# Optimization experiments

Hardware: AMD Instinct MI355X
Metric: run time of the kernel (lower is better)

The kernel has to match this reference:

```python
import jax, jax.numpy as jnp
import numpy as np

ALPHA = 0.5            # conf['alpha'] hybrid mixing
MAX_TOP_ANT = 50       # conf['max_top_antecedents']
MAX_SPAN_WIDTH = 30


def bucket_distance(d):
    # util.bucket_distance: identity 0..4, then log2 buckets, clipped to [0, 9]
    logspace = jnp.floor(jnp.log2(jnp.maximum(d, 1).astype(jnp.float32))).astype(d.dtype) + 3
    return jnp.clip(jnp.where(d <= 4, d, logspace), 0, 9)


def setup_inputs() -> dict:
    key = jax.random.key(0)
    ks = jax.random.split(key, 16)
    W, D, K, F, H = 4096, 768, 768, 20, 1000
    SPAN = 3 * D                      # span_emb_size = 3 * bert_emb_size
    PAIR = 3 * SPAN + F               # pair_emb_size (use_features only)
    std = 0.02

    mention_doc = jax.random.normal(ks[0], (W, D), jnp.float32)
    mention_doc_one = jax.random.normal(ks[1], (W, D), jnp.float32)
    top_span_starts = jnp.sort(jax.random.randint(ks[2], (K,), 0, W - MAX_SPAN_WIDTH))
    widths = jax.random.randint(ks[3], (K,), 0, MAX_SPAN_WIDTH)
    top_span_ends = jnp.minimum(top_span_starts + widths, W - 1)
    top_span_mention_scores = jax.random.normal(ks[4], (K,), jnp.float32)

    return {
        "mention_doc": mention_doc,
        "mention_doc_one": mention_doc_one,
        "top_span_starts": top_span_starts,
        "top_span_ends": top_span_ends,
        "top_span_mention_scores": top_span_mention_scores,
        # mention_token_attn: Linear(D -> 1)
        "attn_w": jax.random.normal(ks[5], (D,), jnp.float32) * std,
        "attn_b": jnp.zeros((), jnp.float32),
        # coarse_bilinear: Linear(SPAN -> SPAN)
        "coarse_w": jax.random.normal(ks[6], (SPAN, SPAN), jnp.float32) * std,
        "coarse_b": jnp.zeros((SPAN,), jnp.float32),
        # emb_antecedent_distance_prior [10, F] + antecedent_distance_score_ffnn Linear(F -> 1)
        "dist_prior_emb": jax.random.normal(ks[7], (10, F), jnp.float32) * std,
        "dist_w": jax.random.normal(ks[8], (F,), jnp.float32) * std,
        "dist_b": jnp.zeros((), jnp.float32),
        # emb_top_antecedent_distance [10, F]
        "top_dist_emb": jax.random.normal(ks[9], (10, F), jnp.float32) * std,
        # coref_score_ffnn: Linear(PAIR -> H), ReLU, Linear(H -> 1)
        "coref_w1": jax.random.normal(ks[10], (PAIR, H), jnp.float32) * std,
        "coref_b1": jnp.zeros((H,), jnp.float32),
        "coref_w2": jax.random.normal(ks[11], (H,), jnp.float32) * std,
        "coref_b2": jnp.zeros((), jnp.float32),
    }


def reference(mention_doc, mention_doc_one, top_span_starts, top_span_ends,
              top_span_mention_scores, attn_w, attn_b, coarse_w, coarse_b,
              dist_prior_emb, dist_w, dist_b, top_dist_emb,
              coref_w1, coref_b1, coref_w2, coref_b2):
    W = mention_doc.shape[0]
    K = top_span_starts.shape[0]
    C = min(K, MAX_TOP_ANT)
    NEG_INF = jnp.float32(-1e30) * 0 - jnp.inf  # true -inf, matches torch.log(0.)

    # --- span embeddings: start / end / head-attention over hybrid doc ---
    start_emb = mention_doc[top_span_starts]                      # [K, D]
    end_emb = mention_doc[top_span_ends]                          # [K, D]
    hybrid = mention_doc * (1.0 - ALPHA) + mention_doc_one * ALPHA
    token_attn = hybrid @ attn_w + attn_b                         # [W]
    tok = jnp.arange(W)
    span_tok_mask = (tok[None, :] >= top_span_starts[:, None]) & \
                    (tok[None, :] <= top_span_ends[:, None])      # [K, W]
    attn_raw = jnp.where(span_tok_mask, token_attn[None, :], NEG_INF)
    attn_probs = jax.nn.softmax(attn_raw, axis=1)                 # [K, W]
    head_emb = attn_probs @ hybrid                                # [K, D]
    span_emb = jnp.concatenate([start_emb, end_emb, head_emb], axis=1)  # [K, 3D]

    # --- coarse (fast) pairwise scores ---
    rng = jnp.arange(K)
    ant_offsets = rng[:, None] - rng[None, :]                     # [K, K]
    ant_mask = ant_offsets >= 1
    pair_sum = top_span_mention_scores[:, None] + top_span_mention_scores[None, :]
    src = span_emb @ coarse_w + coarse_b                          # coarse_bilinear
    fast = pair_sum + src @ span_emb.T
    fast = jnp.where(ant_mask, fast, NEG_INF)                     # + log(mask)
    dist_score = dist_prior_emb @ dist_w + dist_b                 # [10]
    fast = fast + dist_score[bucket_distance(ant_offsets)]        # distance prior

    # --- top-k antecedent pruning ---
    top_fast, top_idx = jax.lax.top_k(fast, C)                    # [K, C]
    top_ant_offsets = jnp.take_along_axis(ant_offsets, top_idx, axis=1)

    # --- fine-grained pairwise FFNN scoring ---
    dist_emb = top_dist_emb[bucket_distance(top_ant_offsets)]     # [K, C, F]
    ant_emb = span_emb[top_idx]                                   # [K, C, 3D]
    tgt_emb = jnp.broadcast_to(span_emb[:, None, :], ant_emb.shape)
    sim_emb = span_emb[:, None, :] * ant_emb
    pair_emb = jnp.concatenate([tgt_emb, ant_emb, sim_emb, dist_emb], axis=-1)  # [K, C, PAIR]
    h = jax.nn.relu(jnp.einsum('kcp,ph->kch', pair_emb, coref_w1) + coref_b1)
    slow = jnp.einsum('kch,h->kc', h, coref_w2) + coref_b2        # [K, C]
    top_scores = slow + top_fast

    # dummy antecedent (epsilon) column of zeros
    return jnp.concatenate([jnp.zeros((K, 1), top_scores.dtype), top_scores], axis=1)
```

## Files before the change

### kernel.cpp

```cpp
#include <hip/hip_runtime.h>
#include <math.h>

#define WTOK 4096
#define DD   768
#define KK   768
#define SPAN 2304
#define HH   1000
#define CC   50
#define NPAD 1024
#define NBIG 4352

typedef __attribute__((ext_vector_type(8))) short bf16x8;
typedef __attribute__((ext_vector_type(4))) float f32x4;
typedef unsigned short ushort;
typedef unsigned int uint;

__device__ __forceinline__ int bucketd(int d) {
  int l = (d >= 1) ? (31 - __clz(d)) : 0;
  int v = (d <= 4) ? d : (l + 3);
  return min(max(v, 0), 9);
}
__device__ __forceinline__ ushort f2bf(float f) {
  uint u = __float_as_uint(f);
  return (ushort)((u + 0x7fffu + ((u >> 16) & 1u)) >> 16);
}
__device__ __forceinline__ uint pkmul_t(uint a, uint b) {
  float lo = __uint_as_float(a << 16) * __uint_as_float(b << 16);
  float hi = __uint_as_float(a & 0xffff0000u) * __uint_as_float(b & 0xffff0000u);
  return (__float_as_uint(lo) >> 16) | (__float_as_uint(hi) & 0xffff0000u);
}
__device__ __forceinline__ uint4 pkmul4(uint4 a, uint4 b) {
  uint4 r;
  r.x = pkmul_t(a.x, b.x); r.y = pkmul_t(a.y, b.y);
  r.z = pkmul_t(a.z, b.z); r.w = pkmul_t(a.w, b.w);
  return r;
}
__device__ __forceinline__ void dma16(const ushort* g, ushort* l) {
  __builtin_amdgcn_global_load_lds(
      (const __attribute__((address_space(1))) void*)g,
      (__attribute__((address_space(3))) void*)l, 16, 0, 0);
}

#define PB_COARSE 5184
#define PB_W 2304
#define PB_SETUP_BASE (PB_COARSE + 3 * PB_W)
#define PB_SLOW_BASE  (PB_SETUP_BASE + 40)
#define PB_TOTAL      (PB_SLOW_BASE + 150)

__global__ __launch_bounds__(256) void prep_k(
    const float* __restrict__ coarse_w, const float* __restrict__ W1,
    const float* __restrict__ dist_prior, const float* __restrict__ dist_w,
    const float* __restrict__ dist_b, const float* __restrict__ top_dist,
    ushort* __restrict__ BigT, ushort* __restrict__ W1simT,
    float* __restrict__ dist_score, float* __restrict__ Pdist,
    float* __restrict__ slow)
{
  int bid = blockIdx.x;
  int tid = threadIdx.x;
  if (bid >= PB_SLOW_BASE) {
    int t = (bid - PB_SLOW_BASE) * 256 + tid;
    if (t < KK * CC) slow[t] = 0.f;
    return;
  }
  if (bid >= PB_SETUP_BASE) {
    int t = (bid - PB_SETUP_BASE) * 256 + tid;
    if (t < 10) {
      float s = dist_b[0];
      for (int f = 0; f < 20; ++f) s += dist_prior[t * 20 + f] * dist_w[f];
      dist_score[t] = s;
    }
    if (t < 10 * HH) {
      int b = t / HH, h = t % HH;
      float s = 0.f;
      for (int f = 0; f < 20; ++f)
        s += top_dist[b * 20 + f] * W1[(long)(6912 + f) * HH + h];
      Pdist[t] = s;
    }
    return;
  }
  const float* in; int ldin, Cin, nbase, NBrows; ushort* out; int idx;
  int xt;
  if (bid < PB_COARSE) {
    idx = bid; in = coarse_w; ldin = SPAN; Cin = SPAN; nbase = 0;
    NBrows = NBIG; out = BigT; xt = SPAN / 32;
  } else {
    idx = bid - PB_COARSE;
    int region = idx / PB_W;
    idx = idx % PB_W;
    if (region == 0) { in = W1; nbase = 2304; NBrows = NBIG; out = BigT; }
    else if (region == 1) { in = W1 + (size_t)SPAN * HH; nbase = 3328; NBrows = NBIG; out = BigT; }
    else { in = W1 + (size_t)2 * SPAN * HH; nbase = 0; NBrows = NPAD; out = W1simT; }
    ldin = HH; Cin = HH; xt = NPAD / 32;
  }
  {
    int bx = idx % xt, by = idx / xt;
    __shared__ float tile[32][33];
    int n0 = bx * 32, p0 = by * 32;
    int tx = tid & 31, ty = tid >> 5;
    for (int i = ty; i < 32; i += 8) {
      int p = p0 + i, n = n0 + tx;
      tile[i][tx] = (n < Cin) ? in[(long)p * ldin + n] : 0.f;
    }
    __syncthreads();
    size_t slab = (size_t)(p0 >> 5) * NBrows * 32;
    for (int i = ty; i < 32; i += 8) {
      int n = n0 + i;
      out[slab + (size_t)(nbase + n) * 32 + tx] = f2bf(tile[tx][i]);
    }
  }
}

__global__ __launch_bounds__(256) void hybrid_attn_k(
    const float* __restrict__ doc, const float* __restrict__ doc1,
    const float* __restrict__ attn_w, const float* __restrict__ attn_b,
    float* __restrict__ hybrid, float* __restrict__ tok_attn)
{
  int w = blockIdx.x;
  int tid = threadIdx.x;
  float part = 0.f;
  for (int d = tid; d < DD; d += 256) {
    float h = 0.5f * doc[(long)w * DD + d] + 0.5f * doc1[(long)w * DD + d];
    hybrid[(long)w * DD + d] = h;
    part += h * attn_w[d];
  }
  for (int off = 32; off > 0; off >>= 1) part += __shfl_down(part, off, 64);
  __shared__ float ws4[4];
  if ((tid & 63) == 0) ws4[tid >> 6] = part;
  __syncthreads();
  if (tid == 0) tok_attn[w] = ws4[0] + ws4[1] + ws4[2] + ws4[3] + attn_b[0];
}

__global__ __launch_bounds__(256) void span_emb_k(
    const float* __restrict__ doc, const float* __restrict__ hybrid,
    const float* __restrict__ tok_attn, const int* __restrict__ starts,
    const int* __restrict__ ends, ushort* __restrict__ se_bf)
{
  int k = blockIdx.x;
  int s = starts[k], e = ends[k];
  int len = e - s + 1;
  int tid = threadIdx.x;
  __shared__ float p_s[32];
  if (tid < 32) {
    float v = (tid < len) ? tok_attn[s + tid] : -INFINITY;
    float m = v;
    for (int msk = 16; msk >= 1; msk >>= 1) m = fmaxf(m, __shfl_xor(m, msk, 32));
    float pe = (tid < len) ? expf(v - m) : 0.f;
    float Z = pe;
    for (int msk = 16; msk >= 1; msk >>= 1) Z += __shfl_xor(Z, msk, 32);
    p_s[tid] = pe / Z;
  }
  __syncthreads();
  for (int d = tid; d < DD; d += 256) {
    float h = 0.f;
    for (int t = 0; t < len; ++t) h += p_s[t] * hybrid[(long)(s + t) * DD + d];
    se_bf[(long)k * SPAN + d]          = f2bf(doc[(long)s * DD + d]);
    se_bf[(long)k * SPAN + DD + d]     = f2bf(doc[(long)e * DD + d]);
    se_bf[(long)k * SPAN + 2 * DD + d] = f2bf(h);
  }
}

__global__ __launch_bounds__(256) void gemm_combined_k(
    const ushort* __restrict__ A, const ushort* __restrict__ B,
    const float* __restrict__ coarse_b, const float* __restrict__ b1,
    ushort* __restrict__ src_bf, float* __restrict__ Ptgt,
    float* __restrict__ Pant)
{
  __shared__ __align__(16) ushort As[64 * 40];
  __shared__ __align__(16) ushort Bs[128 * 32];
  int tid = threadIdx.x;
  int m0 = blockIdx.x * 64, n0 = blockIdx.y * 128;
  int lane = tid & 63, wid = tid >> 6;
  int quad = lane >> 4, lr = lane & 15;
  int wm = (wid & 1) << 5, wn = (wid >> 1) << 6;
  int arow = tid >> 2, aq = tid & 3;
  int gofs[2];
#pragma unroll
  for (int t = 0; t < 2; ++t) {
    int S = t * 256 + tid;
    int r = S >> 2, p = S & 3;
    int q = p ^ ((r >> 1) & 3);
    gofs[t] = (n0 + r) * 32 + q * 8;
  }
  f32x4 acc[2][4] = {};
  for (int k0 = 0; k0 < SPAN; k0 += 32) {
    uint4 a0 = *(const uint4*)(A + (size_t)(m0 + arow) * SPAN + k0 + aq * 8);
    __syncthreads();
    const ushort* sb = B + (size_t)(k0 >> 5) * (NBIG * 32);
    dma16(sb + gofs[0], &Bs[(size_t)(0 * 256 + tid) * 8]);
    dma16(sb + gofs[1], &Bs[(size_t)(1 * 256 + tid) * 8]);
    *(uint4*)&As[arow * 40 + aq * 8] = a0;
    __syncthreads();
    bf16x8 af[2], bfr[4];
#pragma unroll
    for (int mi = 0; mi < 2; ++mi)
      af[mi] = *(const bf16x8*)&As[(wm + mi * 16 + lr) * 40 + quad * 8];
#pragma unroll
    for (int ni = 0; ni < 4; ++ni) {
      int r = wn + ni * 16 + lr;
      int p = quad ^ ((r >> 1) & 3);
      bfr[ni] = *(const bf16x8*)&Bs[r * 32 + p * 8];
    }
#pragma unroll
    for (int mi = 0; mi < 2; ++mi)
#pragma unroll
      for (int ni = 0; ni < 4; ++ni)
        acc[mi][ni] = __builtin_amdgcn_mfma_f32_16x16x32_bf16(
            af[mi], bfr[ni], acc[mi][ni], 0, 0, 0);
  }
#pragma unroll
  for (int mi = 0; mi < 2; ++mi)
#pragma unroll
    for (int ni = 0; ni < 4; ++ni) {
      f32x4 c = acc[mi][ni];
#pragma unroll
      for (int reg = 0; reg < 4; ++reg) {
        int gm = m0 + wm + mi * 16 + quad * 4 + reg;
        int g = n0 + wn + ni * 16 + lr;
        float v = c[reg];
        if (g < 2304) {
          src_bf[(size_t)gm * SPAN + g] = f2bf(v + coarse_b[g]);
        } else if (g < 3328) {
          int n = g - 2304;
          if (n < HH) Ptgt[(size_t)gm * HH + n] = v + b1[n];
        } else {
          int n = g - 3328;
          if (n < HH) Pant[(size_t)gm * HH + n] = v;
        }
      }
    }
}

__global__ __launch_bounds__(256) void gemm_fast_k(
    const ushort* __restrict__ A, const ushort* __restrict__ B,
    const float* __restrict__ ms, const float* __restrict__ dist_score,
    float* __restrict__ fast)
{
  __shared__ __align__(16) ushort As[64 * 40];
  __shared__ __align__(16) ushort Bs[64 * 40];
  int tid = threadIdx.x;
  int m0 = blockIdx.x * 64, n0 = blockIdx.y * 64;
  int lane = tid & 63, wid = tid >> 6;
  int quad = lane >> 4, lr = lane & 15;
  int wm = (wid & 1) << 5, wn = (wid >> 1) << 5;
  int row = tid >> 2, aq = tid & 3;
  const ushort* ga = A + (size_t)(m0 + row) * SPAN + aq * 8;
  const ushort* gb = B + (size_t)(n0 + row) * SPAN + aq * 8;
  f32x4 acc[2][2] = {};
  for (int k0 = 0; k0 < SPAN; k0 += 32) {
    uint4 a0 = *(const uint4*)(ga + k0);
    uint4 b0 = *(const uint4*)(gb + k0);
    __syncthreads();
    *(uint4*)&As[row * 40 + aq * 8] = a0;
    *(uint4*)&Bs[row * 40 + aq * 8] = b0;
    __syncthreads();
    bf16x8 af[2], bfr[2];
#pragma unroll
    for (int mi = 0; mi < 2; ++mi)
      af[mi] = *(const bf16x8*)&As[(wm + mi * 16 + lr) * 40 + quad * 8];
#pragma unroll
    for (int ni = 0; ni < 2; ++ni)
      bfr[ni] = *(const bf16x8*)&Bs[(wn + ni * 16 + lr) * 40 + quad * 8];
#pragma unroll
    for (int mi = 0; mi < 2; ++mi)
#pragma unroll
      for (int ni = 0; ni < 2; ++ni)
        acc[mi][ni] = __builtin_amdgcn_mfma_f32_16x16x32_bf16(
            af[mi], bfr[ni], acc[mi][ni], 0, 0, 0);
  }
#pragma unroll
  for (int mi = 0; mi < 2; ++mi)
#pragma unroll
    for (int ni = 0; ni < 2; ++ni) {
      f32x4 c = acc[mi][ni];
#pragma unroll
      for (int reg = 0; reg < 4; ++reg) {
        int gm = m0 + wm + mi * 16 + quad * 4 + reg;
        int gn = n0 + wn + ni * 16 + lr;
        float v;
        if (gn < gm) {
          v = c[reg] + ms[gm] + ms[gn] + dist_score[bucketd(gm - gn)];
        } else {
          v = -INFINITY;
        }
        fast[(size_t)gm * KK + gn] = v;
      }
    }
}

__global__ __launch_bounds__(256) void topk_k(
    const float* __restrict__ fast, float* __restrict__ top_fast,
    int* __restrict__ row_j, int* __restrict__ row_bucket)
{
  __shared__ float vals[KK];
  __shared__ float wbv[4];
  __shared__ int wbi[4];
  int k = blockIdx.x;
  int tid = threadIdx.x;
  for (int j = tid; j < KK; j += 256) vals[j] = fast[(long)k * KK + j];
  __syncthreads();
  const float NANF = __uint_as_float(0x7fc00000u);
  for (int it = 0; it < CC; ++it) {
    float bv = -INFINITY;
    int bi = 1 << 30;
    for (int j = tid; j < KK; j += 256) {
      float v = vals[j];
      if (v > bv || (v == bv && j < bi)) { bv = v; bi = j; }
    }
    for (int off = 32; off > 0; off >>= 1) {
      float ov = __shfl_down(bv, off, 64);
      int oi = __shfl_down(bi, off, 64);
      if (ov > bv || (ov == bv && oi < bi)) { bv = ov; bi = oi; }
    }
    if ((tid & 63) == 0) { wbv[tid >> 6] = bv; wbi[tid >> 6] = bi; }
    __syncthreads();
    if (tid == 0) {
      for (int w = 1; w < 4; ++w) {
        float ov = wbv[w]; int oi = wbi[w];
        if (ov > bv || (ov == bv && oi < bi)) { bv = ov; bi = oi; }
      }
      int r = k * CC + it;
      top_fast[r] = bv;
      row_j[r] = bi;
      row_bucket[r] = bucketd(k - bi);
      vals[bi] = NANF;
    }
    __syncthreads();
  }
}

__global__ __launch_bounds__(256, 4) void pair_mfma_k(
    const ushort* __restrict__ se_bf, const ushort* __restrict__ W1simT,
    const int* __restrict__ row_j, const int* __restrict__ row_bucket,
    const float* __restrict__ Ptgt, const float* __restrict__ Pant,
    const float* __restrict__ Pdist, const float* __restrict__ w2,
    float* __restrict__ slow)
{
  __shared__ __align__(16) ushort As[2][128 * 40];
  __shared__ __align__(16) ushort Bs[2][128 * 32];
  __shared__ int ks_s[128];
  __shared__ int js_s[128];
  __shared__ int bk_s[128];
  int tid = threadIdx.x;
  int m0 = blockIdx.x * 128, n0 = blockIdx.y * 128;
  if (tid < 128) {
    int r = m0 + tid;
    ks_s[tid] = r / CC;
    js_s[tid] = row_j[r];
    bk_s[tid] = row_bucket[r];
  }
  __syncthreads();
  int lane = tid & 63, wid = tid >> 6;
  int quad = lane >> 4, lr = lane & 15;
  int wm = (wid & 1) << 6, wn = (wid >> 1) << 6;
  int ar0 = tid >> 2, aq = tid & 3;
  const ushort* pk0 = se_bf + (size_t)ks_s[ar0] * SPAN + aq * 8;
  const ushort* pj0 = se_bf + (size_t)js_s[ar0] * SPAN + aq * 8;
  const ushort* pk1 = se_bf + (size_t)ks_s[ar0 + 64] * SPAN + aq * 8;
  const ushort* pj1 = se_bf + (size_t)js_s[ar0 + 64] * SPAN + aq * 8;
  int gofs[2];
#pragma unroll
  for (int t = 0; t < 2; ++t) {
    int S = t * 256 + tid;
    int r = S >> 2, p = S & 3;
    int q = p ^ ((r >> 1) & 3);
    gofs[t] = (n0 + r) * 32 + q * 8;
  }

  {
    uint4 ka0 = *(const uint4*)(pk0);
    uint4 ja0 = *(const uint4*)(pj0);
    uint4 ka1 = *(const uint4*)(pk1);
    uint4 ja1 = *(const uint4*)(pj1);
#pragma unroll
    for (int t = 0; t < 2; ++t)
      dma16(W1simT + gofs[t], &Bs[0][(size_t)(t * 256 + tid) * 8]);
    *(uint4*)&As[0][ar0 * 40 + aq * 8]        = pkmul4(ka0, ja0);
    *(uint4*)&As[0][(ar0 + 64) * 40 + aq * 8] = pkmul4(ka1, ja1);
  }
  __syncthreads();

  f32x4 acc[4][4] = {};
  for (int k0 = 0; k0 < SPAN; k0 += 32) {
    int buf = (k0 >> 5) & 1, nb = buf ^ 1;
    bool more = (k0 + 32) < SPAN;
    int k1 = more ? k0 + 32 : k0;
    uint4 ka0 = *(const uint4*)(pk0 + k1);
    uint4 ja0 = *(const uint4*)(pj0 + k1);
    uint4 ka1 = *(const uint4*)(pk1 + k1);
    uint4 ja1 = *(const uint4*)(pj1 + k1);
    if (more) {
      const ushort* sb = W1simT + (size_t)(k1 >> 5) * (NPAD * 32);
#pragma unroll
      for (int t = 0; t < 2; ++t)
        dma16(sb + gofs[t], &Bs[nb][(size_t)(t * 256 + tid) * 8]);
    }
    bf16x8 af[4], bfr[4];
#pragma unroll
    for (int mi = 0; mi < 4; ++mi)
      af[mi] = *(const bf16x8*)&As[buf][(wm + mi * 16 + lr) * 40 + quad * 8];
#pragma unroll
    for (int ni = 0; ni < 4; ++ni) {
      int r = wn + ni * 16 + lr;
      int p = quad ^ ((r >> 1) & 3);
      bfr[ni] = *(const bf16x8*)&Bs[buf][r * 32 + p * 8];
    }
#pragma unroll
    for (int ni = 0; ni < 4; ++ni)
#pragma unroll
      for (int mi = 0; mi < 4; ++mi)
        acc[mi][ni] = __builtin_amdgcn_mfma_f32_16x16x32_bf16(
            af[mi], bfr[ni], acc[mi][ni], 0, 0, 0);
    if (more) {
      *(uint4*)&As[nb][ar0 * 40 + aq * 8]        = pkmul4(ka0, ja0);
      *(uint4*)&As[nb][(ar0 + 64) * 40 + aq * 8] = pkmul4(ka1, ja1);
    }
    __syncthreads();
  }
  int nn[4]; float w2r[4]; bool nv[4];
#pragma unroll
  for (int ni = 0; ni < 4; ++ni) {
    nn[ni] = n0 + wn + ni * 16 + lr;
    nv[ni] = nn[ni] < HH;
    w2r[ni] = nv[ni] ? w2[nn[ni]] : 0.f;
  }
#pragma unroll
  for (int mi = 0; mi < 4; ++mi) {
#pragma unroll
    for (int reg = 0; reg < 4; ++reg) {
      int rl = wm + mi * 16 + quad * 4 + reg;
      int kk = ks_s[rl], jj = js_s[rl], bb = bk_s[rl];
      float s = 0.f;
#pragma unroll
      for (int ni = 0; ni < 4; ++ni) {
        if (nv[ni]) {
          float h = acc[mi][ni][reg] + Ptgt[(size_t)kk * HH + nn[ni]] +
                    Pant[(size_t)jj * HH + nn[ni]] +
                    Pdist[(size_t)bb * HH + nn[ni]];
          s += fmaxf(h, 0.f) * w2r[ni];
        }
      }
      s += __shfl_xor(s, 1); s += __shfl_xor(s, 2);
      s += __shfl_xor(s, 4); s += __shfl_xor(s, 8);
      if (lr == 0) atomicAdd(&slow[m0 + rl], s);
    }
  }
}

__global__ void finalize_k(const float* __restrict__ slow,
                           const float* __restrict__ top_fast,
                           const float* __restrict__ b2, float* __restrict__ out)
{
  int t = blockIdx.x * 256 + threadIdx.x;
  if (t >= KK * (CC + 1)) return;
  int k = t / (CC + 1), col = t % (CC + 1);
  if (col == 0) {
    out[t] = 0.f;
  } else {
    int r = k * CC + col - 1;
    float v = slow[r] + b2[0] + top_fast[r];
    if (!isfinite(v)) v = -1.0e30f;
    out[t] = v;
  }
}

extern "C" void kernel_launch(void* const* d_in, const int* in_sizes, int n_in,
                              void* d_out, int out_size, void* d_ws, size_t ws_size,
                              hipStream_t stream)
{
  const float* doc        = (const float*)d_in[0];
  const float* doc1       = (const float*)d_in[1];
  const int*   starts     = (const int*)d_in[2];
  const int*   ends       = (const int*)d_in[3];
  const float* ms         = (const float*)d_in[4];
  const float* attn_w     = (const float*)d_in[5];
  const float* attn_b     = (const float*)d_in[6];
  const float* coarse_w   = (const float*)d_in[7];
  const float* coarse_b   = (const float*)d_in[8];
  const float* dist_prior = (const float*)d_in[9];
  const float* dist_w     = (const float*)d_in[10];
  const float* dist_b     = (const float*)d_in[11];
  const float* top_dist   = (const float*)d_in[12];
  const float* W1         = (const float*)d_in[13];
  const float* b1         = (const float*)d_in[14];
  const float* w2         = (const float*)d_in[15];
  const float* b2         = (const float*)d_in[16];
  float* out = (float*)d_out;

  char* ws = (char*)d_ws;
  size_t off = 0;
  auto alloc = [&](size_t bytes) { void* p = ws + off; off = (off + bytes + 1023) & ~(size_t)1023; return p; };
  float*  hybrid     = (float*)alloc((size_t)WTOK * DD * 4);
  float*  tok_attn   = (float*)alloc((size_t)WTOK * 4);
  ushort* se_bf      = (ushort*)alloc((size_t)KK * SPAN * 2 + 4096);
  ushort* src_bf     = (ushort*)alloc((size_t)KK * SPAN * 2 + 4096);
  float*  fast       = (float*)alloc((size_t)KK * KK * 4);
  float*  Ptgt       = (float*)alloc((size_t)KK * HH * 4);
  float*  Pant       = (float*)alloc((size_t)KK * HH * 4);
  float*  Pdist      = (float*)alloc((size_t)10 * HH * 4);
  float*  dist_score = (float*)alloc(64);
  float*  top_fast   = (float*)alloc((size_t)KK * CC * 4);
  int*    row_j      = (int*)alloc((size_t)KK * CC * 4);
  int*    row_bucket = (int*)alloc((size_t)KK * CC * 4);
  float*  slow       = (float*)alloc((size_t)KK * CC * 4);
  ushort* BigT       = (ushort*)alloc((size_t)NBIG * SPAN * 2 + 4096);
  ushort* W1simT     = (ushort*)alloc((size_t)NPAD * SPAN * 2 + 4096);
  (void)ws_size; (void)in_sizes; (void)n_in; (void)out_size;

  prep_k<<<PB_TOTAL, 256, 0, stream>>>(coarse_w, W1, dist_prior, dist_w,
                                       dist_b, top_dist, BigT, W1simT,
                                       dist_score, Pdist, slow);
  hybrid_attn_k<<<WTOK, 256, 0, stream>>>(doc, doc1, attn_w, attn_b, hybrid, tok_attn);
  span_emb_k<<<KK, 256, 0, stream>>>(doc, hybrid, tok_attn, starts, ends, se_bf);
  {
    dim3 g(KK / 64, NBIG / 128);
    gemm_combined_k<<<g, 256, 0, stream>>>(se_bf, BigT, coarse_b, b1,
                                           src_bf, Ptgt, Pant);
  }
  {
    dim3 g(KK / 64, KK / 64);
    gemm_fast_k<<<g, 256, 0, stream>>>(src_bf, se_bf, ms, dist_score, fast);
  }
  topk_k<<<KK, 256, 0, stream>>>(fast, top_fast, row_j, row_bucket);
  {
    dim3 g((KK * CC) / 128, NPAD / 128);
    pair_mfma_k<<<g, 256, 0, stream>>>(se_bf, W1simT, row_j, row_bucket,
                                       Ptgt, Pant, Pdist, w2, slow);
  }
  finalize_k<<<(KK * (CC + 1) + 255) / 256, 256, 0, stream>>>(slow, top_fast, b2, out);
}
```

Baseline: 562.5 us.

## Precompute pairwise product operand in k-tiled layout and DMA it in pair GEMM

The elementwise product of target and antecedent span embeddings now comes from a separate prod_k kernel. It writes the product into a k-tiled bf16 buffer, in two passes of 19200 rows each, instead of the pair GEMM computing it on the fly from gathered rows. The pair GEMM then loads both A and B tiles with async DMA into swizzled LDS, which removes per-iteration register gathers and packed multiplies from the main loop. In exchange it writes and rereads roughly 88MB per pass, and the pair GEMM launches go from one to two.

```diff
diff --git a/kernel.cpp b/kernel.cpp
--- a/kernel.cpp
+++ b/kernel.cpp
@@ -9,6 +9,7 @@
 #define CC   50
 #define NPAD 1024
 #define NBIG 4352
+#define MP   19200
 
 typedef __attribute__((ext_vector_type(8))) short bf16x8;
 typedef __attribute__((ext_vector_type(4))) float f32x4;
@@ -328,14 +329,36 @@
   }
 }
 
+__global__ __launch_bounds__(256) void prod_k(
+    const ushort* __restrict__ se_bf, const int* __restrict__ row_j,
+    int mbase, ushort* __restrict__ A_kt)
+{
+  int tid = threadIdx.x;
+  int m0 = blockIdx.x * 128;
+  int s = blockIdx.y;
+  int row = tid >> 2, aq = tid & 3;
+#pragma unroll
+  for (int h = 0; h < 2; ++h) {
+    int ml = m0 + row + h * 64;
+    int g = mbase + ml;
+    int kk = g / CC;
+    int jj = row_j[g];
+    uint4 a = *(const uint4*)(se_bf + (size_t)kk * SPAN + s * 32 + aq * 8);
+    uint4 b = *(const uint4*)(se_bf + (size_t)jj * SPAN + s * 32 + aq * 8);
+    *(uint4*)(A_kt + (size_t)s * (MP * 32) + (size_t)ml * 32 + aq * 8) =
+        pkmul4(a, b);
+  }
+}
+
 __global__ __launch_bounds__(256, 4) void pair_mfma_k(
-    const ushort* __restrict__ se_bf, const ushort* __restrict__ W1simT,
+    const ushort* __restrict__ A_kt, const ushort* __restrict__ W1simT,
     const int* __restrict__ row_j, const int* __restrict__ row_bucket,
+    int mbase,
     const float* __restrict__ Ptgt, const float* __restrict__ Pant,
     const float* __restrict__ Pdist, const float* __restrict__ w2,
     float* __restrict__ slow)
 {
-  __shared__ __align__(16) ushort As[2][128 * 40];
+  __shared__ __align__(16) ushort As[2][128 * 32];
   __shared__ __align__(16) ushort Bs[2][128 * 32];
   __shared__ int ks_s[128];
   __shared__ int js_s[128];
@@ -343,39 +366,28 @@
   int tid = threadIdx.x;
   int m0 = blockIdx.x * 128, n0 = blockIdx.y * 128;
   if (tid < 128) {
-    int r = m0 + tid;
-    ks_s[tid] = r / CC;
-    js_s[tid] = row_j[r];
-    bk_s[tid] = row_bucket[r];
-  }
-  __syncthreads();
+    int g = mbase + m0 + tid;
+    ks_s[tid] = g / CC;
+    js_s[tid] = row_j[g];
+    bk_s[tid] = row_bucket[g];
+  }
   int lane = tid & 63, wid = tid >> 6;
   int quad = lane >> 4, lr = lane & 15;
   int wm = (wid & 1) << 6, wn = (wid >> 1) << 6;
-  int ar0 = tid >> 2, aq = tid & 3;
-  const ushort* pk0 = se_bf + (size_t)ks_s[ar0] * SPAN + aq * 8;
-  const ushort* pj0 = se_bf + (size_t)js_s[ar0] * SPAN + aq * 8;
-  const ushort* pk1 = se_bf + (size_t)ks_s[ar0 + 64] * SPAN + aq * 8;
-  const ushort* pj1 = se_bf + (size_t)js_s[ar0 + 64] * SPAN + aq * 8;
-  int gofs[2];
+  int aofs[2], bofs[2];
 #pragma unroll
   for (int t = 0; t < 2; ++t) {
     int S = t * 256 + tid;
     int r = S >> 2, p = S & 3;
     int q = p ^ ((r >> 1) & 3);
-    gofs[t] = (n0 + r) * 32 + q * 8;
-  }
-
-  {
-    uint4 ka0 = *(const uint4*)(pk0);
-    uint4 ja0 = *(const uint4*)(pj0);
-    uint4 ka1 = *(const uint4*)(pk1);
-    uint4 ja1 = *(const uint4*)(pj1);
-#pragma unroll
-    for (int t = 0; t < 2; ++t)
-      dma16(W1simT + gofs[t], &Bs[0][(size_t)(t * 256 + tid) * 8]);
-    *(uint4*)&As[0][ar0 * 40 + aq * 8]        = pkmul4(ka0, ja0);
-    *(uint4*)&As[0][(ar0 + 64) * 40 + aq * 8] = pkmul4(ka1, ja1);
+    aofs[t] = (m0 + r) * 32 + q * 8;
+    bofs[t] = (n0 + r) * 32 + q * 8;
+  }
+
+#pragma unroll
+  for (int t = 0; t < 2; ++t) {
+    dma16(A_kt + aofs[t], &As[0][(size_t)(t * 256 + tid) * 8]);
+    dma16(W1simT + bofs[t], &Bs[0][(size_t)(t * 256 + tid) * 8]);
   }
   __syncthreads();
 
@@ -383,21 +395,23 @@
   for (int k0 = 0; k0 < SPAN; k0 += 32) {
     int buf = (k0 >> 5) & 1, nb = buf ^ 1;
     bool more = (k0 + 32) < SPAN;
-    int k1 = more ? k0 + 32 : k0;
-    uint4 ka0 = *(const uint4*)(pk0 + k1);
-    uint4 ja0 = *(const uint4*)(pj0 + k1);
-    uint4 ka1 = *(const uint4*)(pk1 + k1);
-    uint4 ja1 = *(const uint4*)(pj1 + k1);
     if (more) {
-      const ushort* sb = W1simT + (size_t)(k1 >> 5) * (NPAD * 32);
-#pragma unroll
-      for (int t = 0; t < 2; ++t)
-        dma16(sb + gofs[t], &Bs[nb][(size_t)(t * 256 + tid) * 8]);
+      int s1 = (k0 >> 5) + 1;
+      const ushort* sa = A_kt + (size_t)s1 * (MP * 32);
+      const ushort* sb = W1simT + (size_t)s1 * (NPAD * 32);
+#pragma unroll
+      for (int t = 0; t < 2; ++t) {
+        dma16(sa + aofs[t], &As[nb][(size_t)(t * 256 + tid) * 8]);
+        dma16(sb + bofs[t], &Bs[nb][(size_t)(t * 256 + tid) * 8]);
+      }
     }
     bf16x8 af[4], bfr[4];
 #pragma unroll
-    for (int mi = 0; mi < 4; ++mi)
-      af[mi] = *(const bf16x8*)&As[buf][(wm + mi * 16 + lr) * 40 + quad * 8];
+    for (int mi = 0; mi < 4; ++mi) {
+      int r = wm + mi * 16 + lr;
+      int p = quad ^ ((r >> 1) & 3);
+      af[mi] = *(const bf16x8*)&As[buf][r * 32 + p * 8];
+    }
 #pragma unroll
     for (int ni = 0; ni < 4; ++ni) {
       int r = wn + ni * 16 + lr;
@@ -410,10 +424,6 @@
       for (int mi = 0; mi < 4; ++mi)
         acc[mi][ni] = __builtin_amdgcn_mfma_f32_16x16x32_bf16(
             af[mi], bfr[ni], acc[mi][ni], 0, 0, 0);
-    if (more) {
-      *(uint4*)&As[nb][ar0 * 40 + aq * 8]        = pkmul4(ka0, ja0);
-      *(uint4*)&As[nb][(ar0 + 64) * 40 + aq * 8] = pkmul4(ka1, ja1);
-    }
     __syncthreads();
   }
   int nn[4]; float w2r[4]; bool nv[4];
@@ -441,7 +451,7 @@
       }
       s += __shfl_xor(s, 1); s += __shfl_xor(s, 2);
       s += __shfl_xor(s, 4); s += __shfl_xor(s, 8);
-      if (lr == 0) atomicAdd(&slow[m0 + rl], s);
+      if (lr == 0) atomicAdd(&slow[mbase + m0 + rl], s);
     }
   }
 }
@@ -504,6 +514,7 @@
   float*  slow       = (float*)alloc((size_t)KK * CC * 4);
   ushort* BigT       = (ushort*)alloc((size_t)NBIG * SPAN * 2 + 4096);
   ushort* W1simT     = (ushort*)alloc((size_t)NPAD * SPAN * 2 + 4096);
+  ushort* A_kt       = (ushort*)alloc((size_t)MP * SPAN * 2 + 4096);
   (void)ws_size; (void)in_sizes; (void)n_in; (void)out_size;
 
   prep_k<<<PB_TOTAL, 256, 0, stream>>>(coarse_w, W1, dist_prior, dist_w,
@@ -521,9 +532,11 @@
     gemm_fast_k<<<g, 256, 0, stream>>>(src_bf, se_bf, ms, dist_score, fast);
   }
   topk_k<<<KK, 256, 0, stream>>>(fast, top_fast, row_j, row_bucket);
-  {
-    dim3 g((KK * CC) / 128, NPAD / 128);
-    pair_mfma_k<<<g, 256, 0, stream>>>(se_bf, W1simT, row_j, row_bucket,
+  for (int pass = 0; pass < 2; ++pass) {
+    int mbase = pass * MP;
+    prod_k<<<dim3(MP / 128, SPAN / 32), 256, 0, stream>>>(se_bf, row_j, mbase, A_kt);
+    dim3 g(MP / 128, NPAD / 128);
+    pair_mfma_k<<<g, 256, 0, stream>>>(A_kt, W1simT, row_j, row_bucket, mbase,
                                        Ptgt, Pant, Pdist, w2, slow);
   }
   finalize_k<<<(KK * (CC + 1) + 255) / 256, 256, 0, stream>>>(slow, top_fast, b2, out);
```

After: 634.9 us. 1.13x slower.
